# Kernel tuning notes

Hardware: AMD Instinct MI355X
Metric: run time of the kernel (lower is better)

Reference implementation:

```python
import jax, jax.numpy as jnp
import numpy as np

N_NODES = 100000
N_EDGES = 1600000
IN_F = 256
OUT_F = 64
ALPHA = 0.2  # LeakyReLU negative slope


def setup_inputs() -> dict:
    key = jax.random.key(0)
    k1, k2, k3, k4 = jax.random.split(key, 4)
    x = jax.random.normal(k1, (N_NODES, IN_F), dtype=jnp.float32)
    indices = jax.random.randint(k2, (2, N_EDGES), 0, N_NODES, dtype=jnp.int64)
    # xavier_uniform with gain=1.414 ~ U(-b, b), b = gain*sqrt(6/(fan_in+fan_out))
    bW = 1.414 * np.sqrt(6.0 / (IN_F + OUT_F))
    W = jax.random.uniform(k3, (IN_F, OUT_F), dtype=jnp.float32, minval=-bW, maxval=bW)
    ba = 1.414 * np.sqrt(6.0 / (2 * OUT_F + 1))
    a = jax.random.uniform(k4, (2 * OUT_F, 1), dtype=jnp.float32, minval=-ba, maxval=ba)
    return {"x": x, "indices": indices, "W": W, "a": a}


def reference(x, indices, W, a):
    # h = X @ W  -> [N, F_out]
    h = x @ W
    N = h.shape[0]
    src = indices[0]  # segment ids (softmax rows / aggregation targets)
    dst = indices[1]  # gathered neighbor features

    # e_ij = leakyrelu([h_i || h_j] @ a) = leakyrelu(h_i@a1 + h_j@a2)
    # (identical math to concatenation, avoids materializing [E, 2F])
    a1 = a[:OUT_F, 0]
    a2 = a[OUT_F:, 0]
    s1 = h @ a1  # [N]
    s2 = h @ a2  # [N]
    logits = s1[src] + s2[dst]  # [E]
    e = jnp.where(logits > 0, logits, ALPHA * logits)

    # segment softmax over edges grouped by src (sp_softmax)
    m = jax.ops.segment_max(e, src, num_segments=N)
    ex = jnp.exp(e - m[src])
    denom = jax.ops.segment_sum(ex, src, num_segments=N)
    att = ex / denom[src]  # [E]

    # h_prime[i] = sum_j att_ij * h_j  (sp_matmul: weighted scatter-aggregate)
    h_prime = jax.ops.segment_sum(att[:, None] * h[dst], src, num_segments=N)

    # concat=True -> ELU
    return jax.nn.elu(h_prime)
```

## Files before the change

### kernel.cpp

```cpp
#include <hip/hip_runtime.h>
#include <hip/hip_bf16.h>
#include <math.h>

#define NN 100000
#define NE 1600000
#define INF_ 256
#define OF 64

#define NPB 128
#define NB  782
#define CAPB 2560
#define P1B 512
#define CH1 ((NE + P1B - 1) / P1B)
#define OVCAP 8192

constexpr float LRELU_ALPHA = 0.2f;

typedef __attribute__((ext_vector_type(8))) short short8;
typedef __attribute__((ext_vector_type(4))) float f32x4;

static __device__ __forceinline__ unsigned short f2bf(float f) {
    union { float f; unsigned int u; } v; v.f = f;
    unsigned int r = v.u + 0x7fff + ((v.u >> 16) & 1);
    return (unsigned short)(r >> 16);
}
static __device__ __forceinline__ float bf2f(unsigned short b) {
    union { unsigned int u; float f; } v; v.u = ((unsigned int)b) << 16;
    return v.f;
}
static __device__ __forceinline__ unsigned int pkbf(float a, float b) {
    union { __hip_bfloat162 h; unsigned int u; } c;
    c.h = __float22bfloat162_rn(make_float2(a, b));
    return c.u;
}

union S8 { short8 s; unsigned int u[4]; };

__global__ __launch_bounds__(256) void k_prep(const float* __restrict__ W,
                                              const float* __restrict__ a,
                                              float* __restrict__ wa) {
    int r = threadIdx.x;
    float t1 = 0.f, t2 = 0.f;
#pragma unroll 8
    for (int c = 0; c < OF; ++c) {
        float w = W[r * OF + c];
        t1 += w * a[c];
        t2 += w * a[OF + c];
    }
    wa[r] = t1;
    wa[256 + r] = t2;
}

__global__ __launch_bounds__(256) void k_gemm_mfma(const float* __restrict__ x,
                                                   const float* __restrict__ W,
                                                   const float* __restrict__ wa,
                                                   unsigned short* __restrict__ h,
                                                   float* __restrict__ s1,
                                                   float* __restrict__ s2) {
    __shared__ short Wf[2560 * 8];
    int tid = threadIdx.x;
    for (int i = tid; i < 2560; i += 256) {
        int ks = i / 320;
        int rem = i - ks * 320;
        int ct = rem >> 6;
        int l  = rem & 63;
        int kb = ks * 32 + ((l >> 4) << 3);
        int c  = l & 15;
        S8 v;
        if (ct < 4) {
            int col = ct * 16 + c;
#pragma unroll
            for (int j = 0; j < 4; ++j)
                v.u[j] = pkbf(W[(size_t)(kb + 2 * j) * OF + col],
                              W[(size_t)(kb + 2 * j + 1) * OF + col]);
        } else if (c < 2) {
            const float* src = wa + c * 256;
#pragma unroll
            for (int j = 0; j < 4; ++j)
                v.u[j] = pkbf(src[kb + 2 * j], src[kb + 2 * j + 1]);
        } else {
#pragma unroll
            for (int j = 0; j < 4; ++j) v.u[j] = 0u;
        }
        ((short8*)Wf)[i] = v.s;
    }
    __syncthreads();

    int wid = tid >> 6, lane = tid & 63;
    int rowbase = blockIdx.x * 128 + wid * 32;
    int r0 = rowbase + (lane & 15);
    int koff = (lane >> 4) << 3;

    f32x4 acc[2][5];
#pragma unroll
    for (int rt = 0; rt < 2; ++rt)
#pragma unroll
        for (int ct = 0; ct < 5; ++ct) acc[rt][ct] = (f32x4){0.f, 0.f, 0.f, 0.f};

#pragma unroll 1
    for (int ks = 0; ks < 8; ++ks) {
        S8 af[2];
#pragma unroll
        for (int rt = 0; rt < 2; ++rt) {
            int r = r0 + rt * 16;
            if (r < NN) {
                const float* p = x + (size_t)r * INF_ + ks * 32 + koff;
                float4 xa = *(const float4*)p;
                float4 xb = *(const float4*)(p + 4);
                af[rt].u[0] = pkbf(xa.x, xa.y);
                af[rt].u[1] = pkbf(xa.z, xa.w);
                af[rt].u[2] = pkbf(xb.x, xb.y);
                af[rt].u[3] = pkbf(xb.z, xb.w);
            } else {
#pragma unroll
                for (int j = 0; j < 4; ++j) af[rt].u[j] = 0u;
            }
        }
#pragma unroll
        for (int rt = 0; rt < 2; ++rt)
#pragma unroll
            for (int ct = 0; ct < 5; ++ct)
                acc[rt][ct] = __builtin_amdgcn_mfma_f32_16x16x32_bf16(
                    af[rt].s, ((short8*)Wf)[(ks * 5 + ct) * 64 + lane], acc[rt][ct], 0, 0, 0);
    }

    int c = lane & 15, rowq = lane >> 4;
#pragma unroll
    for (int rt = 0; rt < 2; ++rt) {
#pragma unroll
        for (int reg = 0; reg < 4; ++reg) {
            int r = rowbase + rt * 16 + rowq * 4 + reg;
            if (r < NN) {
#pragma unroll
                for (int ct = 0; ct < 4; ++ct)
                    h[(size_t)r * OF + ct * 16 + c] = f2bf(acc[rt][ct][reg]);
                float sv = acc[rt][4][reg];
                if (c == 0)      s1[r] = sv;
                else if (c == 1) s2[r] = sv;
            }
        }
    }
}

__global__ __launch_bounds__(256) void k_part1(const int* __restrict__ idx,
                                               int* __restrict__ cur_b,
                                               int* __restrict__ pairs,
                                               int2* __restrict__ ov_list) {
    __shared__ int hist[NB];
    __shared__ int gbase[NB];
    int tid = threadIdx.x, blk = blockIdx.x;
    for (int i = tid; i < NB; i += 256) hist[i] = 0;
    __syncthreads();
    int e0 = blk * CH1, e1 = min(e0 + CH1, NE);
    for (int e = e0 + tid; e < e1; e += 256)
        atomicAdd(&hist[idx[e] >> 7], 1);
    __syncthreads();
    for (int i = tid; i < NB; i += 256) {
        int c = hist[i];
        gbase[i] = c ? atomicAdd(&cur_b[i], c) : 0;
        hist[i] = 0;
    }
    __syncthreads();
    for (int e = e0 + tid; e < e1; e += 256) {
        int s = idx[e], d = idx[NE + e];
        int b = s >> 7;
        int p = gbase[b] + atomicAdd(&hist[b], 1);
        if (p < CAPB) pairs[b * CAPB + p] = ((s & 127) << 17) | d;
        else {
            int j = atomicAdd(&cur_b[NB], 1);
            if (j < OVCAP) ov_list[j] = make_int2(s, d);
        }
    }
}

__global__ __launch_bounds__(256) void k_part2(const int* __restrict__ pairs,
                                               const int* __restrict__ cur_b,
                                               const int2* __restrict__ ov_list,
                                               int* __restrict__ start,
                                               int* __restrict__ deg,
                                               int* __restrict__ sorted_dst) {
    __shared__ int stage[CAPB + 128];
    __shared__ int cnt[NPB], pfx[NPB];
    __shared__ int extra;
    int tid = threadIdx.x, b = blockIdx.x;
    if (tid < NPB) cnt[tid] = 0;
    if (tid == 0) extra = 0;
    __syncthreads();

    int t_b = cur_b[b];
    int nin = min(t_b, CAPB);
    for (int i = tid; i < nin; i += 256) {
        int v = pairs[b * CAPB + i];
        stage[i] = v;
        atomicAdd(&cnt[v >> 17], 1);
    }
    if (t_b > CAPB) {
        int ovn = min(cur_b[NB], OVCAP);
        for (int i = tid; i < ovn; i += 256) {
            int2 e = ov_list[i];
            if ((e.x >> 7) == b) {
                int k = atomicAdd(&extra, 1);
                if (k < 128) {
                    stage[CAPB + k] = ((e.x & 127) << 17) | e.y;
                    atomicAdd(&cnt[e.x & 127], 1);
                }
            }
        }
    }
    __syncthreads();
    int ntot = nin + min(extra, 128);

    if (tid < NPB) pfx[tid] = cnt[tid];
    __syncthreads();
    for (int off = 1; off < NPB; off <<= 1) {
        int xv = (tid >= off && tid < NPB) ? pfx[tid - off] : 0;
        __syncthreads();
        if (tid < NPB) pfx[tid] += xv;
        __syncthreads();
    }
    if (tid < NPB) {
        int ex = pfx[tid] - cnt[tid];
        int g = b * NPB + tid;
        if (g < NN) { start[g] = b * CAPB + ex; deg[g] = cnt[tid]; }
        cnt[tid] = ex;
    }
    __syncthreads();
    for (int i = tid; i < ntot; i += 256) {
        int v = stage[i];
        int p = atomicAdd(&cnt[v >> 17], 1);
        sorted_dst[b * CAPB + p] = v & 0x1FFFF;
    }
}

__global__ __launch_bounds__(256) void k_agg(const int* __restrict__ sorted_dst,
                                             const int* __restrict__ start,
                                             const int* __restrict__ deg,
                                             const float* __restrict__ s1,
                                             const float* __restrict__ s2,
                                             const unsigned short* __restrict__ h,
                                             float* __restrict__ out) {
    __shared__ int2 tile[4][64];
    int tid = threadIdx.x;
    int wid = tid >> 6, lane = tid & 63;
    int node = blockIdx.x * 4 + wid;
    if (node >= NN) return;

    int st = start[node];
    int dg = deg[node];
    float s1n = s1[node];
    float den = 0.f, acc = 0.f;

    for (int base = 0; base < dg; base += 64) {
        int cnt = min(64, dg - base);
        int dj = 0; float exj = 0.f;
        if (lane < cnt) {
            dj = sorted_dst[st + base + lane];
            float lg = s1n + s2[dj];
            float el = lg > 0.f ? lg : LRELU_ALPHA * lg;
            exj = expf(el);
        }
        tile[wid][lane] = make_int2(dj, __float_as_int(exj));
        asm volatile("s_waitcnt lgkmcnt(0)" ::: "memory");
#pragma unroll 4
        for (int j = 0; j < cnt; ++j) {
            int2 pr = tile[wid][j];
            float e = __int_as_float(pr.y);
            den += e;
            acc += e * bf2f(h[(size_t)pr.x * OF + lane]);
        }
        asm volatile("" ::: "memory");
    }

    float inv = den > 0.f ? 1.f / den : 0.f;
    float v = acc * inv;
    out[(size_t)node * OF + lane] = v > 0.f ? v : expf(v) - 1.f;
}

extern "C" void kernel_launch(void* const* d_in, const int* in_sizes, int n_in,
                              void* d_out, int out_size, void* d_ws, size_t ws_size,
                              hipStream_t stream) {
    const float* x   = (const float*)d_in[0];
    const int*   idx = (const int*)d_in[1];
    const float* W   = (const float*)d_in[2];
    const float* a   = (const float*)d_in[3];
    float* out = (float*)d_out;

    char* ws = (char*)d_ws;
    unsigned short* h = (unsigned short*)ws;  ws += sizeof(unsigned short) * (size_t)NN * OF;
    int*  pairs       = (int*)ws;             ws += sizeof(int) * (size_t)NB * CAPB;
    int*  sorted_dst  = (int*)ws;             ws += sizeof(int) * (size_t)NB * CAPB;
    float* s1         = (float*)ws;           ws += sizeof(float) * NN;
    float* s2         = (float*)ws;           ws += sizeof(float) * NN;
    int*   start      = (int*)ws;             ws += sizeof(int) * NN;
    int*   deg        = (int*)ws;             ws += sizeof(int) * NN;
    int*   cur_b      = (int*)ws;             ws += sizeof(int) * (NB + 16);
    int2*  ov_list    = (int2*)ws;            ws += sizeof(int2) * OVCAP;
    float* wa         = (float*)ws;           ws += sizeof(float) * 512;

    hipMemsetAsync(cur_b, 0, sizeof(int) * (NB + 16), stream);
    k_prep<<<1, 256, 0, stream>>>(W, a, wa);
    k_gemm_mfma<<<(NN + 127) / 128, 256, 0, stream>>>(x, W, wa, h, s1, s2);
    k_part1<<<P1B, 256, 0, stream>>>(idx, cur_b, pairs, ov_list);
    k_part2<<<NB, 256, 0, stream>>>(pairs, cur_b, ov_list, start, deg, sorted_dst);
    k_agg<<<(NN + 3) / 4, 256, 0, stream>>>(sorted_dst, start, deg, s1, s2, h, out);
}
```

Baseline: 295.2 us.

## Fuse prep, GEMM and partition into one launch; fuse sort with aggregation

Merges the W·a precompute into each GEMM block and runs the GEMM and the edge-partition pass as disjoint block ranges of one kernel so they can overlap. The second partition stage now sorts edges into shared memory, computes the attention exponentials there and aggregates directly, which drops the sorted_dst/start/deg round trip and one launch. The cost is that aggregation parallelism falls from one wave per node to 782 blocks that each loop over 32 nodes per wave with half-wave edge splits, which may reduce latency hiding on the random h gathers. Every GEMM block also recomputes the W·a vectors redundantly.

```diff
diff --git a/kernel.cpp b/kernel.cpp
--- a/kernel.cpp
+++ b/kernel.cpp
@@ -10,6 +10,8 @@
 #define NPB 128
 #define NB  782
 #define CAPB 2560
+#define ED (CAPB + 128)
+#define GEMMB 782
 #define P1B 512
 #define CH1 ((NE + P1B - 1) / P1B)
 #define OVCAP 8192
@@ -36,154 +38,167 @@
 
 union S8 { short8 s; unsigned int u[4]; };
 
-__global__ __launch_bounds__(256) void k_prep(const float* __restrict__ W,
-                                              const float* __restrict__ a,
-                                              float* __restrict__ wa) {
-    int r = threadIdx.x;
-    float t1 = 0.f, t2 = 0.f;
+__global__ __launch_bounds__(256) void k_fused1(const float* __restrict__ x,
+                                                const float* __restrict__ W,
+                                                const float* __restrict__ a,
+                                                const int* __restrict__ idx,
+                                                int* __restrict__ cur_b,
+                                                int* __restrict__ pairs,
+                                                int2* __restrict__ ov_list,
+                                                unsigned short* __restrict__ h,
+                                                float* __restrict__ s1,
+                                                float* __restrict__ s2) {
+    __shared__ __align__(16) char smem[43008];
+    int tid = threadIdx.x;
+
+    if (blockIdx.x < GEMMB) {
+        short* Wf  = (short*)smem;
+        float* wal = (float*)(smem + 40960);
+
+        {
+            float t1 = 0.f, t2 = 0.f;
+            const float* wr = W + tid * OF;
 #pragma unroll 8
-    for (int c = 0; c < OF; ++c) {
-        float w = W[r * OF + c];
-        t1 += w * a[c];
-        t2 += w * a[OF + c];
-    }
-    wa[r] = t1;
-    wa[256 + r] = t2;
-}
-
-__global__ __launch_bounds__(256) void k_gemm_mfma(const float* __restrict__ x,
-                                                   const float* __restrict__ W,
-                                                   const float* __restrict__ wa,
-                                                   unsigned short* __restrict__ h,
-                                                   float* __restrict__ s1,
-                                                   float* __restrict__ s2) {
-    __shared__ short Wf[2560 * 8];
-    int tid = threadIdx.x;
-    for (int i = tid; i < 2560; i += 256) {
-        int ks = i / 320;
-        int rem = i - ks * 320;
-        int ct = rem >> 6;
-        int l  = rem & 63;
-        int kb = ks * 32 + ((l >> 4) << 3);
-        int c  = l & 15;
-        S8 v;
-        if (ct < 4) {
-            int col = ct * 16 + c;
-#pragma unroll
-            for (int j = 0; j < 4; ++j)
-                v.u[j] = pkbf(W[(size_t)(kb + 2 * j) * OF + col],
-                              W[(size_t)(kb + 2 * j + 1) * OF + col]);
-        } else if (c < 2) {
-            const float* src = wa + c * 256;
-#pragma unroll
-            for (int j = 0; j < 4; ++j)
-                v.u[j] = pkbf(src[kb + 2 * j], src[kb + 2 * j + 1]);
-        } else {
-#pragma unroll
-            for (int j = 0; j < 4; ++j) v.u[j] = 0u;
-        }
-        ((short8*)Wf)[i] = v.s;
-    }
-    __syncthreads();
-
-    int wid = tid >> 6, lane = tid & 63;
-    int rowbase = blockIdx.x * 128 + wid * 32;
-    int r0 = rowbase + (lane & 15);
-    int koff = (lane >> 4) << 3;
-
-    f32x4 acc[2][5];
-#pragma unroll
-    for (int rt = 0; rt < 2; ++rt)
-#pragma unroll
-        for (int ct = 0; ct < 5; ++ct) acc[rt][ct] = (f32x4){0.f, 0.f, 0.f, 0.f};
+            for (int c = 0; c < OF; ++c) {
+                float w = wr[c];
+                t1 += w * a[c];
+                t2 += w * a[OF + c];
+            }
+            wal[tid] = t1;
+            wal[256 + tid] = t2;
+        }
+        __syncthreads();
+
+        for (int i = tid; i < 2560; i += 256) {
+            int ks = i / 320;
+            int rem = i - ks * 320;
+            int ct = rem >> 6;
+            int l  = rem & 63;
+            int kb = ks * 32 + ((l >> 4) << 3);
+            int c  = l & 15;
+            S8 v;
+            if (ct < 4) {
+                int col = ct * 16 + c;
+#pragma unroll
+                for (int j = 0; j < 4; ++j)
+                    v.u[j] = pkbf(W[(size_t)(kb + 2 * j) * OF + col],
+                                  W[(size_t)(kb + 2 * j + 1) * OF + col]);
+            } else if (c < 2) {
+                const float* src = wal + c * 256;
+#pragma unroll
+                for (int j = 0; j < 4; ++j)
+                    v.u[j] = pkbf(src[kb + 2 * j], src[kb + 2 * j + 1]);
+            } else {
+#pragma unroll
+                for (int j = 0; j < 4; ++j) v.u[j] = 0u;
+            }
+            ((short8*)Wf)[i] = v.s;
+        }
+        __syncthreads();
+
+        int wid = tid >> 6, lane = tid & 63;
+        int rowbase = blockIdx.x * 128 + wid * 32;
+        int r0 = rowbase + (lane & 15);
+        int koff = (lane >> 4) << 3;
+
+        f32x4 acc[2][5];
+#pragma unroll
+        for (int rt = 0; rt < 2; ++rt)
+#pragma unroll
+            for (int ct = 0; ct < 5; ++ct) acc[rt][ct] = (f32x4){0.f, 0.f, 0.f, 0.f};
 
 #pragma unroll 1
-    for (int ks = 0; ks < 8; ++ks) {
-        S8 af[2];
+        for (int ks = 0; ks < 8; ++ks) {
+            S8 af[2];
+#pragma unroll
+            for (int rt = 0; rt < 2; ++rt) {
+                int r = r0 + rt * 16;
+                if (r < NN) {
+                    const float* p = x + (size_t)r * INF_ + ks * 32 + koff;
+                    float4 xa = *(const float4*)p;
+                    float4 xb = *(const float4*)(p + 4);
+                    af[rt].u[0] = pkbf(xa.x, xa.y);
+                    af[rt].u[1] = pkbf(xa.z, xa.w);
+                    af[rt].u[2] = pkbf(xb.x, xb.y);
+                    af[rt].u[3] = pkbf(xb.z, xb.w);
+                } else {
+#pragma unroll
+                    for (int j = 0; j < 4; ++j) af[rt].u[j] = 0u;
+                }
+            }
+#pragma unroll
+            for (int rt = 0; rt < 2; ++rt)
+#pragma unroll
+                for (int ct = 0; ct < 5; ++ct)
+                    acc[rt][ct] = __builtin_amdgcn_mfma_f32_16x16x32_bf16(
+                        af[rt].s, ((short8*)Wf)[(ks * 5 + ct) * 64 + lane], acc[rt][ct], 0, 0, 0);
+        }
+
+        int c = lane & 15, rowq = lane >> 4;
 #pragma unroll
         for (int rt = 0; rt < 2; ++rt) {
-            int r = r0 + rt * 16;
-            if (r < NN) {
-                const float* p = x + (size_t)r * INF_ + ks * 32 + koff;
-                float4 xa = *(const float4*)p;
-                float4 xb = *(const float4*)(p + 4);
-                af[rt].u[0] = pkbf(xa.x, xa.y);
-                af[rt].u[1] = pkbf(xa.z, xa.w);
-                af[rt].u[2] = pkbf(xb.x, xb.y);
-                af[rt].u[3] = pkbf(xb.z, xb.w);
-            } else {
-#pragma unroll
-                for (int j = 0; j < 4; ++j) af[rt].u[j] = 0u;
-            }
-        }
-#pragma unroll
-        for (int rt = 0; rt < 2; ++rt)
-#pragma unroll
-            for (int ct = 0; ct < 5; ++ct)
-                acc[rt][ct] = __builtin_amdgcn_mfma_f32_16x16x32_bf16(
-                    af[rt].s, ((short8*)Wf)[(ks * 5 + ct) * 64 + lane], acc[rt][ct], 0, 0, 0);
-    }
-
-    int c = lane & 15, rowq = lane >> 4;
-#pragma unroll
-    for (int rt = 0; rt < 2; ++rt) {
-#pragma unroll
-        for (int reg = 0; reg < 4; ++reg) {
-            int r = rowbase + rt * 16 + rowq * 4 + reg;
-            if (r < NN) {
-#pragma unroll
-                for (int ct = 0; ct < 4; ++ct)
-                    h[(size_t)r * OF + ct * 16 + c] = f2bf(acc[rt][ct][reg]);
-                float sv = acc[rt][4][reg];
-                if (c == 0)      s1[r] = sv;
-                else if (c == 1) s2[r] = sv;
-            }
-        }
-    }
-}
-
-__global__ __launch_bounds__(256) void k_part1(const int* __restrict__ idx,
-                                               int* __restrict__ cur_b,
-                                               int* __restrict__ pairs,
-                                               int2* __restrict__ ov_list) {
-    __shared__ int hist[NB];
-    __shared__ int gbase[NB];
-    int tid = threadIdx.x, blk = blockIdx.x;
-    for (int i = tid; i < NB; i += 256) hist[i] = 0;
-    __syncthreads();
-    int e0 = blk * CH1, e1 = min(e0 + CH1, NE);
-    for (int e = e0 + tid; e < e1; e += 256)
-        atomicAdd(&hist[idx[e] >> 7], 1);
-    __syncthreads();
-    for (int i = tid; i < NB; i += 256) {
-        int c = hist[i];
-        gbase[i] = c ? atomicAdd(&cur_b[i], c) : 0;
-        hist[i] = 0;
-    }
-    __syncthreads();
-    for (int e = e0 + tid; e < e1; e += 256) {
-        int s = idx[e], d = idx[NE + e];
-        int b = s >> 7;
-        int p = gbase[b] + atomicAdd(&hist[b], 1);
-        if (p < CAPB) pairs[b * CAPB + p] = ((s & 127) << 17) | d;
-        else {
-            int j = atomicAdd(&cur_b[NB], 1);
-            if (j < OVCAP) ov_list[j] = make_int2(s, d);
-        }
-    }
-}
-
-__global__ __launch_bounds__(256) void k_part2(const int* __restrict__ pairs,
-                                               const int* __restrict__ cur_b,
-                                               const int2* __restrict__ ov_list,
-                                               int* __restrict__ start,
-                                               int* __restrict__ deg,
-                                               int* __restrict__ sorted_dst) {
-    __shared__ int stage[CAPB + 128];
-    __shared__ int cnt[NPB], pfx[NPB];
+#pragma unroll
+            for (int reg = 0; reg < 4; ++reg) {
+                int r = rowbase + rt * 16 + rowq * 4 + reg;
+                if (r < NN) {
+#pragma unroll
+                    for (int ct = 0; ct < 4; ++ct)
+                        h[(size_t)r * OF + ct * 16 + c] = f2bf(acc[rt][ct][reg]);
+                    float sv = acc[rt][4][reg];
+                    if (c == 0)      s1[r] = sv;
+                    else if (c == 1) s2[r] = sv;
+                }
+            }
+        }
+    } else {
+        int blk = blockIdx.x - GEMMB;
+        int* hist  = (int*)smem;
+        int* gbase = (int*)smem + NB;
+        for (int i = tid; i < NB; i += 256) hist[i] = 0;
+        __syncthreads();
+        int e0 = blk * CH1, e1 = min(e0 + CH1, NE);
+        for (int e = e0 + tid; e < e1; e += 256)
+            atomicAdd(&hist[idx[e] >> 7], 1);
+        __syncthreads();
+        for (int i = tid; i < NB; i += 256) {
+            int c = hist[i];
+            gbase[i] = c ? atomicAdd(&cur_b[i], c) : 0;
+            hist[i] = 0;
+        }
+        __syncthreads();
+        for (int e = e0 + tid; e < e1; e += 256) {
+            int s = idx[e], d = idx[NE + e];
+            int b = s >> 7;
+            int p = gbase[b] + atomicAdd(&hist[b], 1);
+            if (p < CAPB) pairs[b * CAPB + p] = ((s & 127) << 17) | d;
+            else {
+                int j = atomicAdd(&cur_b[NB], 1);
+                if (j < OVCAP) ov_list[j] = make_int2(s, d);
+            }
+        }
+    }
+}
+
+__global__ __launch_bounds__(256) void k_fused2(const int* __restrict__ pairs,
+                                                const int* __restrict__ cur_b,
+                                                const int2* __restrict__ ov_list,
+                                                const float* __restrict__ s1,
+                                                const float* __restrict__ s2,
+                                                const unsigned short* __restrict__ h,
+                                                float* __restrict__ out) {
+    __shared__ int  stage[ED];
+    __shared__ int2 el[ED];
+    __shared__ int cnt[NPB], pfx[NPB], cur[NPB];
+    __shared__ float s1l[NPB];
     __shared__ int extra;
     int tid = threadIdx.x, b = blockIdx.x;
-    if (tid < NPB) cnt[tid] = 0;
+    int node0 = b * NPB;
+
+    if (tid < NPB) {
+        cnt[tid] = 0;
+        int g = node0 + tid;
+        s1l[tid] = (g < NN) ? s1[g] : 0.f;
+    }
     if (tid == 0) extra = 0;
     __syncthreads();
 
@@ -218,62 +233,51 @@
         if (tid < NPB) pfx[tid] += xv;
         __syncthreads();
     }
-    if (tid < NPB) {
-        int ex = pfx[tid] - cnt[tid];
-        int g = b * NPB + tid;
-        if (g < NN) { start[g] = b * CAPB + ex; deg[g] = cnt[tid]; }
-        cnt[tid] = ex;
-    }
-    __syncthreads();
+    if (tid < NPB) cur[tid] = pfx[tid] - cnt[tid];
+    __syncthreads();
+
     for (int i = tid; i < ntot; i += 256) {
         int v = stage[i];
-        int p = atomicAdd(&cnt[v >> 17], 1);
-        sorted_dst[b * CAPB + p] = v & 0x1FFFF;
-    }
-}
-
-__global__ __launch_bounds__(256) void k_agg(const int* __restrict__ sorted_dst,
-                                             const int* __restrict__ start,
-                                             const int* __restrict__ deg,
-                                             const float* __restrict__ s1,
-                                             const float* __restrict__ s2,
-                                             const unsigned short* __restrict__ h,
-                                             float* __restrict__ out) {
-    __shared__ int2 tile[4][64];
-    int tid = threadIdx.x;
+        int ls = v >> 17;
+        int p = atomicAdd(&cur[ls], 1);
+        el[p] = make_int2(v & 0x1FFFF, ls);
+    }
+    __syncthreads();
+
+    for (int i = tid; i < ntot; i += 256) {
+        int2 e = el[i];
+        float lg = s1l[e.y] + s2[e.x];
+        float elr = lg > 0.f ? lg : LRELU_ALPHA * lg;
+        el[i].y = __float_as_int(expf(elr));
+    }
+    __syncthreads();
+
     int wid = tid >> 6, lane = tid & 63;
-    int node = blockIdx.x * 4 + wid;
-    if (node >= NN) return;
-
-    int st = start[node];
-    int dg = deg[node];
-    float s1n = s1[node];
-    float den = 0.f, acc = 0.f;
-
-    for (int base = 0; base < dg; base += 64) {
-        int cnt = min(64, dg - base);
-        int dj = 0; float exj = 0.f;
-        if (lane < cnt) {
-            dj = sorted_dst[st + base + lane];
-            float lg = s1n + s2[dj];
-            float el = lg > 0.f ? lg : LRELU_ALPHA * lg;
-            exj = expf(el);
-        }
-        tile[wid][lane] = make_int2(dj, __float_as_int(exj));
-        asm volatile("s_waitcnt lgkmcnt(0)" ::: "memory");
-#pragma unroll 4
-        for (int j = 0; j < cnt; ++j) {
-            int2 pr = tile[wid][j];
-            float e = __int_as_float(pr.y);
-            den += e;
-            acc += e * bf2f(h[(size_t)pr.x * OF + lane]);
-        }
-        asm volatile("" ::: "memory");
-    }
-
-    float inv = den > 0.f ? 1.f / den : 0.f;
-    float v = acc * inv;
-    out[(size_t)node * OF + lane] = v > 0.f ? v : expf(v) - 1.f;
+    int half = lane >> 5, f2 = lane & 31;
+    for (int ln = wid * 32; ln < wid * 32 + 32; ++ln) {
+        int node = node0 + ln;
+        if (node >= NN) break;
+        int dg = cnt[ln];
+        int st = pfx[ln] - dg;
+        float den = 0.f, ax = 0.f, ay = 0.f;
+        for (int j = half; j < dg; j += 2) {
+            int2 e = el[st + j];
+            float ex = __int_as_float(e.y);
+            den += ex;
+            unsigned int hv = *(const unsigned int*)(h + (size_t)e.x * OF + f2 * 2);
+            ax += ex * bf2f((unsigned short)(hv & 0xFFFFu));
+            ay += ex * bf2f((unsigned short)(hv >> 16));
+        }
+        den += __shfl_xor(den, 32, 64);
+        ax  += __shfl_xor(ax, 32, 64);
+        ay  += __shfl_xor(ay, 32, 64);
+        float inv = den > 0.f ? 1.f / den : 0.f;
+        float vx = ax * inv, vy = ay * inv;
+        vx = vx > 0.f ? vx : expf(vx) - 1.f;
+        vy = vy > 0.f ? vy : expf(vy) - 1.f;
+        if (half == 0)
+            *(float2*)(out + (size_t)node * OF + f2 * 2) = make_float2(vx, vy);
+    }
 }
 
 extern "C" void kernel_launch(void* const* d_in, const int* in_sizes, int n_in,
@@ -288,19 +292,12 @@
     char* ws = (char*)d_ws;
     unsigned short* h = (unsigned short*)ws;  ws += sizeof(unsigned short) * (size_t)NN * OF;
     int*  pairs       = (int*)ws;             ws += sizeof(int) * (size_t)NB * CAPB;
-    int*  sorted_dst  = (int*)ws;             ws += sizeof(int) * (size_t)NB * CAPB;
     float* s1         = (float*)ws;           ws += sizeof(float) * NN;
     float* s2         = (float*)ws;           ws += sizeof(float) * NN;
-    int*   start      = (int*)ws;             ws += sizeof(int) * NN;
-    int*   deg        = (int*)ws;             ws += sizeof(int) * NN;
     int*   cur_b      = (int*)ws;             ws += sizeof(int) * (NB + 16);
     int2*  ov_list    = (int2*)ws;            ws += sizeof(int2) * OVCAP;
-    float* wa         = (float*)ws;           ws += sizeof(float) * 512;
 
     hipMemsetAsync(cur_b, 0, sizeof(int) * (NB + 16), stream);
-    k_prep<<<1, 256, 0, stream>>>(W, a, wa);
-    k_gemm_mfma<<<(NN + 127) / 128, 256, 0, stream>>>(x, W, wa, h, s1, s2);
-    k_part1<<<P1B, 256, 0, stream>>>(idx, cur_b, pairs, ov_list);
-    k_part2<<<NB, 256, 0, stream>>>(pairs, cur_b, ov_list, start, deg, sorted_dst);
-    k_agg<<<(NN + 3) / 4, 256, 0, stream>>>(sorted_dst, start, deg, s1, s2, h, out);
-}
+    k_fused1<<<GEMMB + P1B, 256, 0, stream>>>(x, W, a, idx, cur_b, pairs, ov_list, h, s1, s2);
+    k_fused2<<<NB, 256, 0, stream>>>(pairs, cur_b, ov_list, s1, s2, h, out);
+}
```

Result: slower. 343.4 us (+16.3%).
